# Optimization experiments

Hardware: AMD Instinct MI355X
Metric: run time of the kernel (lower is better)

Reference implementation:

```python
import jax, jax.numpy as jnp
import numpy as np
import math

N = 256          # DFT size
B = 262144       # number of frames (batch)


def _dft_matrix(n):
    # W[r, c] = exp(-2j*pi/n) ** (r*c)
    rc = np.outer(np.arange(n), np.arange(n))
    W = np.exp(-2j * np.pi * rc / n)
    return W


def setup_inputs() -> dict:
    key = jax.random.key(0)
    k1, k2 = jax.random.split(key)
    x_real = jax.random.normal(k1, (B, N), dtype=jnp.float32)
    x_imag = jax.random.normal(k2, (B, N), dtype=jnp.float32)
    W = _dft_matrix(N)
    W_real = jnp.asarray(np.real(W), dtype=jnp.float32)
    W_imag = jnp.asarray(np.imag(W), dtype=jnp.float32)
    return {"x_real": x_real, "x_imag": x_imag, "W_real": W_real, "W_imag": W_imag}


def reference(x_real, x_imag, W_real, W_imag):
    # complex_mul via 4 real matmuls, then normal=True epilogue scale 1/sqrt(n)
    real = jnp.matmul(x_real, W_real) - jnp.matmul(x_imag, W_imag)
    imag = jnp.matmul(x_real, W_imag) + jnp.matmul(x_imag, W_real)
    scale = 1.0 / math.sqrt(N)
    return (real * scale, imag * scale)
```

## Files before the change

kernel.cpp:

```cpp
#include <hip/hip_runtime.h>
#include <math.h>

#define FS 264

__device__ __forceinline__ void dft16(float* xr, float* xi) {
  constexpr float TWR[10] = {1.f, 0.9238795325f, 0.7071067812f, 0.3826834324f, 0.f,
                             -0.3826834324f, -0.7071067812f, -0.9238795325f, -1.f,
                             -0.9238795325f};
  constexpr float TWI[10] = {0.f, -0.3826834324f, -0.7071067812f, -0.9238795325f, -1.f,
                             -0.9238795325f, -0.7071067812f, -0.3826834324f, 0.f,
                             0.3826834324f};
  float yr[16], yi[16];
#pragma unroll
  for (int b = 0; b < 4; ++b) {
    float x0r = xr[b],      x0i = xi[b];
    float x1r = xr[b + 4],  x1i = xi[b + 4];
    float x2r = xr[b + 8],  x2i = xi[b + 8];
    float x3r = xr[b + 12], x3i = xi[b + 12];
    float t0r = x0r + x2r, t0i = x0i + x2i;
    float t1r = x0r - x2r, t1i = x0i - x2i;
    float t2r = x1r + x3r, t2i = x1i + x3i;
    float t3r = x1r - x3r, t3i = x1i - x3i;
    yr[0 + b]  = t0r + t2r;  yi[0 + b]  = t0i + t2i;
    yr[8 + b]  = t0r - t2r;  yi[8 + b]  = t0i - t2i;
    yr[4 + b]  = t1r + t3i;  yi[4 + b]  = t1i - t3r;
    yr[12 + b] = t1r - t3i;  yi[12 + b] = t1i + t3r;
  }
#pragma unroll
  for (int c = 0; c < 4; ++c) {
    float zr[4], zi[4];
#pragma unroll
    for (int b = 0; b < 4; ++b) {
      const int k = b * c;
      float ar = yr[c * 4 + b], ai = yi[c * 4 + b];
      zr[b] = ar * TWR[k] - ai * TWI[k];
      zi[b] = ar * TWI[k] + ai * TWR[k];
    }
    float t0r = zr[0] + zr[2], t0i = zi[0] + zi[2];
    float t1r = zr[0] - zr[2], t1i = zi[0] - zi[2];
    float t2r = zr[1] + zr[3], t2i = zi[1] + zi[3];
    float t3r = zr[1] - zr[3], t3i = zi[1] - zi[3];
    xr[c]      = t0r + t2r;  xi[c]      = t0i + t2i;
    xr[c + 8]  = t0r - t2r;  xi[c + 8]  = t0i - t2i;
    xr[c + 4]  = t1r + t3i;  xi[c + 4]  = t1i - t3r;
    xr[c + 12] = t1r - t3i;  xi[c + 12] = t1i + t3r;
  }
}

__global__ __launch_bounds__(256, 4) void dft256_kernel(
    const float* __restrict__ xr, const float* __restrict__ xi,
    float* __restrict__ out, size_t half) {
  __shared__ __align__(16) float sA[16 * FS];
  __shared__ __align__(16) float sB[16 * FS];
  const int t = threadIdx.x;
  const size_t blk_off = (size_t)blockIdx.x * 4096;

  const float4* xr4 = (const float4*)(xr + blk_off);
  const float4* xi4 = (const float4*)(xi + blk_off);
  float4* sA4 = (float4*)sA;
  float4* sB4 = (float4*)sB;
#pragma unroll
  for (int i = 0; i < 4; ++i) {
    int g = t + (i << 8);
    int l = (g >> 6) * 66 + (g & 63);
    sA4[l] = xr4[g];
    sB4[l] = xi4[g];
  }
  __syncthreads();

  const int f = t >> 4;
  const int b = t & 15;
  const int fb = f * FS;

  float vr[16], vi[16];
#pragma unroll
  for (int a = 0; a < 16; ++a) {
    vr[a] = sA[fb + a * 16 + b];
    vi[a] = sB[fb + a * 16 + b];
  }
  dft16(vr, vi);

  float swb, cwb;
  __sincosf(-6.283185307179586f * (float)b * (1.0f / 256.0f), &swb, &cwb);
  float twr = 1.f, twi = 0.f;
#pragma unroll
  for (int c = 0; c < 16; ++c) {
    float ar = vr[c], ai = vi[c];
    vr[c] = ar * twr - ai * twi;
    vi[c] = ar * twi + ai * twr;
    float ntr = twr * cwb - twi * swb;
    twi = twr * swb + twi * cwb;
    twr = ntr;
  }
  __syncthreads();

#pragma unroll
  for (int c = 0; c < 16; ++c) {
    sA[fb + c * 16 + b] = vr[c];
    sB[fb + c * 16 + b] = vi[c];
  }
  __syncthreads();

  {
    const int base = fb + b * 16;
#pragma unroll
    for (int j = 0; j < 4; ++j) {
      float4 r  = *(const float4*)&sA[base + 4 * j];
      float4 im = *(const float4*)&sB[base + 4 * j];
      vr[4 * j + 0] = r.x;  vr[4 * j + 1] = r.y;  vr[4 * j + 2] = r.z;  vr[4 * j + 3] = r.w;
      vi[4 * j + 0] = im.x; vi[4 * j + 1] = im.y; vi[4 * j + 2] = im.z; vi[4 * j + 3] = im.w;
    }
  }
  dft16(vr, vi);
  __syncthreads();

#pragma unroll
  for (int d = 0; d < 16; ++d) {
    sA[fb + d * 16 + b] = vr[d] * 0.0625f;
    sB[fb + d * 16 + b] = vi[d] * 0.0625f;
  }
  __syncthreads();

  float4* outr4 = (float4*)(out + blk_off);
  float4* outi4 = (float4*)(out + half + blk_off);
#pragma unroll
  for (int i = 0; i < 4; ++i) {
    int g = t + (i << 8);
    int l = (g >> 6) * 66 + (g & 63);
    outr4[g] = sA4[l];
    outi4[g] = sB4[l];
  }
}

extern "C" void kernel_launch(void* const* d_in, const int* in_sizes, int n_in,
                              void* d_out, int out_size, void* d_ws, size_t ws_size,
                              hipStream_t stream) {
  const float* xr = (const float*)d_in[0];
  const float* xi = (const float*)d_in[1];
  float* out = (float*)d_out;
  const size_t half = (size_t)in_sizes[0];
  const int blocks = (int)(half / 4096);
  dft256_kernel<<<blocks, 256, 0, stream>>>(xr, xi, out, half);
}
```

Measured before the change: 835.0 us.

## Drop LDS staging and block barriers; use wave-local exchange with direct strided I/O

The kernel now loads each thread's 16 strided elements straight from global memory and stores results straight back, using nontemporal loads and stores instead of staging through shared memory with float4 copies. The transpose between the two radix-16 passes uses one shared buffer, done first for the real part and then for the imaginary part. It relies on each 16-thread frame group sitting inside one wavefront, so it uses s_waitcnt in place of __syncthreads. This removes four block-wide barriers, halves LDS use (which may raise occupancy) and drops two LDS round trips. The cost is global accesses coalesced in 64-byte segments rather than full float4 rows, and a dependence on wave64 execution for correctness.

```diff
diff --git a/kernel.cpp b/kernel.cpp
--- a/kernel.cpp
+++ b/kernel.cpp
@@ -50,34 +50,21 @@
 __global__ __launch_bounds__(256, 4) void dft256_kernel(
     const float* __restrict__ xr, const float* __restrict__ xi,
     float* __restrict__ out, size_t half) {
-  __shared__ __align__(16) float sA[16 * FS];
-  __shared__ __align__(16) float sB[16 * FS];
+  __shared__ __align__(16) float s[16 * FS];
   const int t = threadIdx.x;
-  const size_t blk_off = (size_t)blockIdx.x * 4096;
-
-  const float4* xr4 = (const float4*)(xr + blk_off);
-  const float4* xi4 = (const float4*)(xi + blk_off);
-  float4* sA4 = (float4*)sA;
-  float4* sB4 = (float4*)sB;
-#pragma unroll
-  for (int i = 0; i < 4; ++i) {
-    int g = t + (i << 8);
-    int l = (g >> 6) * 66 + (g & 63);
-    sA4[l] = xr4[g];
-    sB4[l] = xi4[g];
-  }
-  __syncthreads();
-
   const int f = t >> 4;
   const int b = t & 15;
-  const int fb = f * FS;
+  const size_t frame = (size_t)blockIdx.x * 16 + f;
 
+  const float* gr = xr + frame * 256 + b;
+  const float* gi = xi + frame * 256 + b;
   float vr[16], vi[16];
 #pragma unroll
   for (int a = 0; a < 16; ++a) {
-    vr[a] = sA[fb + a * 16 + b];
-    vi[a] = sB[fb + a * 16 + b];
+    vr[a] = __builtin_nontemporal_load(gr + a * 16);
+    vi[a] = __builtin_nontemporal_load(gi + a * 16);
   }
+
   dft16(vr, vi);
 
   float swb, cwb;
@@ -92,43 +79,38 @@
     twi = twr * swb + twi * cwb;
     twr = ntr;
   }
-  __syncthreads();
 
+  const int fb = f * FS;
+  const int rbase = fb + b * 16;
+  float ur[16], ui[16];
 #pragma unroll
-  for (int c = 0; c < 16; ++c) {
-    sA[fb + c * 16 + b] = vr[c];
-    sB[fb + c * 16 + b] = vi[c];
+  for (int c = 0; c < 16; ++c) s[fb + c * 16 + b] = vr[c];
+  asm volatile("s_waitcnt lgkmcnt(0)" ::: "memory");
+#pragma unroll
+  for (int j = 0; j < 4; ++j) {
+    float4 q = *(const float4*)&s[rbase + 4 * j];
+    ur[4 * j + 0] = q.x; ur[4 * j + 1] = q.y;
+    ur[4 * j + 2] = q.z; ur[4 * j + 3] = q.w;
   }
-  __syncthreads();
+  asm volatile("s_waitcnt lgkmcnt(0)" ::: "memory");
+#pragma unroll
+  for (int c = 0; c < 16; ++c) s[fb + c * 16 + b] = vi[c];
+  asm volatile("s_waitcnt lgkmcnt(0)" ::: "memory");
+#pragma unroll
+  for (int j = 0; j < 4; ++j) {
+    float4 q = *(const float4*)&s[rbase + 4 * j];
+    ui[4 * j + 0] = q.x; ui[4 * j + 1] = q.y;
+    ui[4 * j + 2] = q.z; ui[4 * j + 3] = q.w;
+  }
 
-  {
-    const int base = fb + b * 16;
-#pragma unroll
-    for (int j = 0; j < 4; ++j) {
-      float4 r  = *(const float4*)&sA[base + 4 * j];
-      float4 im = *(const float4*)&sB[base + 4 * j];
-      vr[4 * j + 0] = r.x;  vr[4 * j + 1] = r.y;  vr[4 * j + 2] = r.z;  vr[4 * j + 3] = r.w;
-      vi[4 * j + 0] = im.x; vi[4 * j + 1] = im.y; vi[4 * j + 2] = im.z; vi[4 * j + 3] = im.w;
-    }
-  }
-  dft16(vr, vi);
-  __syncthreads();
+  dft16(ur, ui);
 
+  float* go_r = out + frame * 256 + b;
+  float* go_i = out + half + frame * 256 + b;
 #pragma unroll
   for (int d = 0; d < 16; ++d) {
-    sA[fb + d * 16 + b] = vr[d] * 0.0625f;
-    sB[fb + d * 16 + b] = vi[d] * 0.0625f;
-  }
-  __syncthreads();
-
-  float4* outr4 = (float4*)(out + blk_off);
-  float4* outi4 = (float4*)(out + half + blk_off);
-#pragma unroll
-  for (int i = 0; i < 4; ++i) {
-    int g = t + (i << 8);
-    int l = (g >> 6) * 66 + (g & 63);
-    outr4[g] = sA4[l];
-    outi4[g] = sB4[l];
+    __builtin_nontemporal_store(ur[d] * 0.0625f, go_r + d * 16);
+    __builtin_nontemporal_store(ui[d] * 0.0625f, go_i + d * 16);
   }
 }
 
```

Measured after the change: 848.7 us. No clear change (+1.6%).
